# Kernel optimization log

Hardware: AMD Instinct MI355X
Metric: run time of the kernel (lower is better)

Reference implementation:

```python
import jax, jax.numpy as jnp
import numpy as np

EPS = 1e-12  # F.normalize eps


def setup_inputs() -> dict:
    key = jax.random.key(0)
    k1, k2 = jax.random.split(key)
    bs, d = 8192, 128
    data = jax.random.normal(k1, (bs, d), dtype=jnp.float32)
    label = jax.random.randint(k2, (bs, 1), 0, 2, dtype=jnp.int64)
    scale = jnp.asarray(np.log(1.0 / 0.07), dtype=jnp.float32)  # learned temperature param
    return {"data": data, "scale": scale, "label": label}


def reference(data, scale, label):
    bs = data.shape[0]
    # L2-normalize rows (F.normalize semantics with eps clamp)
    norm = jnp.maximum(jnp.linalg.norm(data, axis=-1, keepdims=True), EPS)
    x = data / norm
    logits = (x @ x.T) * jnp.exp(scale)  # [bs, bs]
    # Vectorized equivalent of the python double loop: binary same-class matrix
    sim = (label == label.T).astype(logits.dtype)  # [bs, bs]
    q = jax.nn.softmax(sim / jnp.sum(sim, axis=-1, keepdims=True), axis=-1)
    p = jax.nn.log_softmax(logits, axis=-1)
    log_q = jnp.log(q)  # q > 0 always (softmax output)
    # F.kl_div(p, q, 'batchmean') = sum(q * (log q - p)) / bs
    loss1 = jnp.sum(q * (log_q - p)) / bs
    # F.kl_div(q.log(), p.exp(), 'batchmean') = sum(exp(p) * (p - log q)) / bs
    loss2 = jnp.sum(jnp.exp(p) * (p - log_q)) / bs
    return (loss1 + loss2) * 0.5
```

## Files before the change

kernel.cpp:

```cpp
#include <hip/hip_runtime.h>
#include <stdint.h>

#define BS 8192
#define DD 128
#define L2E 1.4426950408889634f
#define LN2 0.6931471805599453f

typedef __attribute__((ext_vector_type(8))) short short8;
typedef __attribute__((ext_vector_type(4))) float float4v;

#if __has_builtin(__builtin_amdgcn_exp2f)
#define EXP2(x) __builtin_amdgcn_exp2f(x)
#else
#define EXP2(x) exp2f(x)
#endif

__device__ __forceinline__ float bf2f(short s) {
  union { unsigned u; float f; } c;
  c.u = ((unsigned)(unsigned short)s) << 16;
  return c.f;
}
__device__ __forceinline__ short f2bf(float f) {
  union { float f; unsigned u; } c; c.f = f;
  unsigned u = c.u + 0x7FFFu + ((c.u >> 16) & 1u);
  return (short)(u >> 16);
}


__global__ __launch_bounds__(256) void k_norm(const float* __restrict__ data,
                                              const int* __restrict__ label,
                                              char* __restrict__ xnbF,
                                              float* __restrict__ gh16,
                                              float* __restrict__ Zr,
                                              float* __restrict__ Ur,
                                              float* __restrict__ Vr,
                                              float* __restrict__ mf) {
  __shared__ float shg[256];
  int tid = threadIdx.x, wave = tid >> 6, lane = tid & 63;
  int lh = lane & 31, rsel = lane >> 5;
  shg[tid] = 0.f;
  int rowbase = blockIdx.x * 16;
  if (tid < 16) {
    int row = rowbase + tid;
    Zr[row] = 0.f; Ur[row] = 0.f; Vr[row] = 0.f;
    mf[row] = (label[row] == 0) ? 1.f : 0.f;
  }
  __syncthreads();

  float a00 = 0.f, a01 = 0.f, a02 = 0.f, a03 = 0.f;
  float a10 = 0.f, a11 = 0.f, a12 = 0.f, a13 = 0.f;
#pragma unroll
  for (int it = 0; it < 2; ++it) {
    int row = rowbase + it * 8 + wave * 2 + rsel;
    float4 v = *(const float4*)&data[row * DD + lh * 4];
    float ss = v.x * v.x + v.y * v.y + v.z * v.z + v.w * v.w;
#pragma unroll
    for (int off = 16; off; off >>= 1) ss += __shfl_xor(ss, off);
    float rn = 1.f / fmaxf(sqrtf(ss), 1e-12f);
    float x0 = v.x * rn, x1 = v.y * rn, x2 = v.z * rn, x3 = v.w * rn;

    unsigned pk0 = (unsigned)(unsigned short)f2bf(x0) |
                   ((unsigned)(unsigned short)f2bf(x1) << 16);
    unsigned pk1 = (unsigned)(unsigned short)f2bf(x2) |
                   ((unsigned)(unsigned short)f2bf(x3) << 16);
    int kc = lh >> 1;
    size_t chunk = (size_t)(row >> 4) * 256 + (size_t)(kc >> 2) * 64 +
                   (size_t)(kc & 3) * 16 + (row & 15);
    *(uint2*)(xnbF + chunk * 16 + (lh & 1) * 8) = make_uint2(pk0, pk1);

    int lab = label[row];
    if (lab == 0) {
      a00 += x0; a01 += x1; a02 += x2; a03 += x3;
    } else {
      a10 += x0; a11 += x1; a12 += x2; a13 += x3;
    }
  }
  int base = lh * 4;
  atomicAdd(&shg[base + 0], a00); atomicAdd(&shg[base + 1], a01);
  atomicAdd(&shg[base + 2], a02); atomicAdd(&shg[base + 3], a03);
  atomicAdd(&shg[128 + base + 0], a10); atomicAdd(&shg[128 + base + 1], a11);
  atomicAdd(&shg[128 + base + 2], a12); atomicAdd(&shg[128 + base + 3], a13);
  __syncthreads();
  atomicAdd(&gh16[(blockIdx.x & 15) * 256 + tid], shg[tid]);
}

__global__ __launch_bounds__(512, 4) void k_main(const short* __restrict__ xnbF,
                                                 const int* __restrict__ label,
                                                 const float* __restrict__ mf,
                                                 const float* __restrict__ scale,
                                                 const float* __restrict__ gh16,
                                                 float* __restrict__ Zr,
                                                 float* __restrict__ Ur,
                                                 float* __restrict__ Vr,
                                                 int* __restrict__ ticket,
                                                 float* __restrict__ out) {
  __shared__ short tile[2][64 * DD];
  __shared__ int credu[8];
  __shared__ float fredu[8];
  __shared__ float dred[24];
  __shared__ int lastf;
  int tid = threadIdx.x, wave = tid >> 6, lane = tid & 63;
  int quad = lane >> 4, col = lane & 15;
  int rbI = blockIdx.x >> 4;
  int sl = blockIdx.x & 15;
  float se2 = __expf(scale[0]) * L2E;

  const short8* F = (const short8*)xnbF;
  int gA = rbI * 16 + wave * 2;
  short8 af[2][4];
#pragma unroll
  for (int s = 0; s < 2; ++s)
#pragma unroll
    for (int t = 0; t < 4; ++t) {
      short8 a = F[(size_t)(gA + s) * 256 + t * 64 + lane];
#pragma unroll
      for (int i = 0; i < 8; ++i) a[i] = f2bf(bf2f(a[i]) * se2);
      af[s][t] = a;
    }

  float4v Z0 = {0.f,0.f,0.f,0.f}, Z1 = Z0, U0 = Z0, U1 = Z0, V0 = Z0, V1 = Z0;
  int cb4 = sl * 32;

#define STAGE(buf, jt)                                                         \
  {                                                                            \
    const char* s_ = (const char*)xnbF +                                       \
                     ((size_t)(cb4 + (jt) * 4) * 256 + tid) * 16;              \
    char* d_ = (char*)tile[buf] + tid * 16;                                    \
    __builtin_amdgcn_global_load_lds(                                          \
        (const __attribute__((address_space(1))) void*)(uintptr_t)s_,          \
        (__attribute__((address_space(3))) void*)(uintptr_t)d_, 16, 0, 0);     \
    __builtin_amdgcn_global_load_lds(                                          \
        (const __attribute__((address_space(1))) void*)(uintptr_t)(s_ + 8192), \
        (__attribute__((address_space(3))) void*)(uintptr_t)(d_ + 8192),       \
        16, 0, 0);                                                             \
  }

  STAGE(0, 0);
  __syncthreads();

#pragma unroll 1
  for (int jt = 0; jt < 8; ++jt) {
    if (jt < 7) STAGE((jt + 1) & 1, jt + 1);
    const short8* T8 = (const short8*)tile[jt & 1];
    int jcb = sl * 512 + jt * 64;

#define HALFTILE(jo)                                                           \
    {                                                                          \
      short8 b00 = T8[(jo) * 256 + lane];                                      \
      short8 b01 = T8[(jo) * 256 + 64 + lane];                                 \
      short8 b02 = T8[(jo) * 256 + 128 + lane];                                \
      short8 b03 = T8[(jo) * 256 + 192 + lane];                                \
      short8 b10 = T8[(jo + 1) * 256 + lane];                                  \
      short8 b11 = T8[(jo + 1) * 256 + 64 + lane];                             \
      short8 b12 = T8[(jo + 1) * 256 + 128 + lane];                            \
      short8 b13 = T8[(jo + 1) * 256 + 192 + lane];                            \
      float m0 = mf[jcb + (jo) * 16 + col];                                    \
      float m1 = mf[jcb + (jo + 1) * 16 + col];                                \
      float4v c00 = {0.f, 0.f, 0.f, 0.f}, c01 = c00, c10 = c00, c11 = c00;     \
      c00 = __builtin_amdgcn_mfma_f32_16x16x32_bf16(af[0][0], b00, c00, 0,0,0);\
      c01 = __builtin_amdgcn_mfma_f32_16x16x32_bf16(af[1][0], b00, c01, 0,0,0);\
      c10 = __builtin_amdgcn_mfma_f32_16x16x32_bf16(af[0][0], b10, c10, 0,0,0);\
      c11 = __builtin_amdgcn_mfma_f32_16x16x32_bf16(af[1][0], b10, c11, 0,0,0);\
      c00 = __builtin_amdgcn_mfma_f32_16x16x32_bf16(af[0][1], b01, c00, 0,0,0);\
      c01 = __builtin_amdgcn_mfma_f32_16x16x32_bf16(af[1][1], b01, c01, 0,0,0);\
      c10 = __builtin_amdgcn_mfma_f32_16x16x32_bf16(af[0][1], b11, c10, 0,0,0);\
      c11 = __builtin_amdgcn_mfma_f32_16x16x32_bf16(af[1][1], b11, c11, 0,0,0);\
      c00 = __builtin_amdgcn_mfma_f32_16x16x32_bf16(af[0][2], b02, c00, 0,0,0);\
      c01 = __builtin_amdgcn_mfma_f32_16x16x32_bf16(af[1][2], b02, c01, 0,0,0);\
      c10 = __builtin_amdgcn_mfma_f32_16x16x32_bf16(af[0][2], b12, c10, 0,0,0);\
      c11 = __builtin_amdgcn_mfma_f32_16x16x32_bf16(af[1][2], b12, c11, 0,0,0);\
      c00 = __builtin_amdgcn_mfma_f32_16x16x32_bf16(af[0][3], b03, c00, 0,0,0);\
      c01 = __builtin_amdgcn_mfma_f32_16x16x32_bf16(af[1][3], b03, c01, 0,0,0);\
      c10 = __builtin_amdgcn_mfma_f32_16x16x32_bf16(af[0][3], b13, c10, 0,0,0);\
      c11 = __builtin_amdgcn_mfma_f32_16x16x32_bf16(af[1][3], b13, c11, 0,0,0);\
      _Pragma("unroll")                                                        \
      for (int r = 0; r < 4; ++r) {  \
        float l, e;                                                            \
        l = c00[r]; e = EXP2(l);        \
        Z0[r] += e; U0[r] = fmaf(e, l, U0[r]); V0[r] = fmaf(m0, e, V0[r]);     \
        l = c01[r]; e = EXP2(l);                                               \
        Z1[r] += e; U1[r] = fmaf(e, l, U1[r]); V1[r] = fmaf(m0, e, V1[r]);     \
        l = c10[r]; e = EXP2(l);                                               \
        Z0[r] += e; U0[r] = fmaf(e, l, U0[r]); V0[r] = fmaf(m1, e, V0[r]);     \
        l = c11[r]; e = EXP2(l);                                               \
        Z1[r] += e; U1[r] = fmaf(e, l, U1[r]); V1[r] = fmaf(m1, e, V1[r]);     \
      }                                                                        \
    }
    HALFTILE(0)
    HALFTILE(2)
#undef HALFTILE
    __syncthreads();
  }
#undef STAGE

#define EMIT(s, Zc, Uc, Vc)                                                    \
  {                                                                            \
    _Pragma("unroll")                                                          \
    for (int r = 0; r < 4; ++r) {                                              \
      float z = Zc[r], u = Uc[r], v0 = Vc[r];                                  \
      _Pragma("unroll")                                                        \
      for (int off = 1; off < 16; off <<= 1) {                                 \
        z += __shfl_xor(z, off);                                               \
        u += __shfl_xor(u, off);                                               \
        v0 += __shfl_xor(v0, off);                                             \
      }                                                                        \
      if (col == 0) {                                                          \
        int row = rbI * 256 + wave * 32 + s * 16 + quad * 4 + r;               \
        int lab = label[row];                                                  \
        float v = (lab == 0) ? v0 : (z - v0);                                  \
        atomicAdd(&Zr[row], z);                                                \
        atomicAdd(&Ur[row], u * LN2);                 \
        atomicAdd(&Vr[row], v);                                                \
      }                                                                        \
    }                                                                          \
  }
  EMIT(0, Z0, U0, V0)
  EMIT(1, Z1, U1, V1)
#undef EMIT

  __syncthreads();
  if (tid == 0) {
    int t = __hip_atomic_fetch_add(ticket, 1, __ATOMIC_ACQ_REL,
                                   __HIP_MEMORY_SCOPE_AGENT);
    lastf = (t == 511);
  }
  __syncthreads();
  if (!lastf) return;

  float* hs = (float*)tile;
  if (tid < 256) {
    float h = 0.f;
#pragma unroll
    for (int i = 0; i < 16; ++i) h += gh16[i * 256 + tid];
    hs[tid] = h;
  }
  int c1i = 0;
#pragma unroll
  for (int k = 0; k < 16; ++k) c1i += label[k * 512 + tid];
#pragma unroll
  for (int off = 32; off; off >>= 1) c1i += __shfl_xor(c1i, off);
  if (lane == 0) credu[wave] = c1i;
  __syncthreads();
  int c1t = 0;
#pragma unroll
  for (int w = 0; w < 8; ++w) c1t += credu[w];
  float c1 = (float)c1t, c0 = (float)(BS - c1t);

  float p00 = 0.f, p01 = 0.f, p11 = 0.f;
  if (tid < 128) {
    float h0d = hs[tid], h1d = hs[128 + tid];
    p00 = h0d * h0d; p01 = h0d * h1d; p11 = h1d * h1d;
  }
#pragma unroll
  for (int off = 32; off; off >>= 1) {
    p00 += __shfl_xor(p00, off);
    p01 += __shfl_xor(p01, off);
    p11 += __shfl_xor(p11, off);
  }
  if (lane == 0) { dred[wave] = p00; dred[8 + wave] = p01; dred[16 + wave] = p11; }

  float rc0 = 1.f / c0, rc1 = 1.f / c1;
  float local = 0.f;
#pragma unroll
  for (int k = 0; k < 16; ++k) {
    int row = k * 512 + tid;
    int lab = label[row];
    float Z = __hip_atomic_load(&Zr[row], __ATOMIC_RELAXED, __HIP_MEMORY_SCOPE_AGENT);
    float U = __hip_atomic_load(&Ur[row], __ATOMIC_RELAXED, __HIP_MEMORY_SCOPE_AGENT);
    float V = __hip_atomic_load(&Vr[row], __ATOMIC_RELAXED, __HIP_MEMORY_SCOPE_AGENT);
    local += (U - V * (lab ? rc1 : rc0)) / Z;
  }
#pragma unroll
  for (int off = 32; off; off >>= 1) local += __shfl_xor(local, off);
  if (lane == 0) fredu[wave] = local;
  __syncthreads();
  if (tid == 0) {
    float se = __expf(scale[0]);
    float a0 = __expf(1.f / c0), a1 = __expf(1.f / c1);
    float rZq0 = 1.f / (c0 * a0 + ((float)BS - c0));
    float rZq1 = 1.f / (c1 * a1 + ((float)BS - c1));
    float d00 = dred[0] + dred[1], d01 = dred[8] + dred[9],
          d11 = dred[16] + dred[17];
    float rows = 0.f;
#pragma unroll
    for (int w = 0; w < 8; ++w) rows += fredu[w];
    float stsum = se * (rZq0 * ((d00 + d01) + (a0 - 1.f) * d00) +
                        rZq1 * ((d01 + d11) + (a1 - 1.f) * d11));
    float total = c0 * a0 * rZq0 + c1 * a1 * rZq1 - stsum + rows;
    out[0] = total * (0.5f / (float)BS);
  }
}

extern "C" void kernel_launch(void* const* d_in, const int* in_sizes, int n_in,
                              void* d_out, int out_size, void* d_ws, size_t ws_size,
                              hipStream_t stream) {
  const float* data = (const float*)d_in[0];
  const float* scale = (const float*)d_in[1];
  const int* label = (const int*)d_in[2];
  char* ws = (char*)d_ws;
  char* xnbF = ws;
  float* Zr = (float*)(ws + 2097152);
  float* Ur = (float*)(ws + 2129920);
  float* Vr = (float*)(ws + 2162688);
  float* gh16 = (float*)(ws + 2195456);
  int* ticket = (int*)(ws + 2211840);
  float* mf = (float*)(ws + 2211872);

  hipMemsetAsync(ws + 2195456, 0, 16388, stream);

  k_norm<<<512, 256, 0, stream>>>(data, label, xnbF, gh16, Zr, Ur, Vr, mf);
  k_main<<<512, 512, 0, stream>>>((const short*)xnbF, label, mf, scale, gh16,
                                  Zr, Ur, Vr, ticket, (float*)d_out);
}
```

Measured before the change: 102.9 us.

## Replace memset and ticket-based last-block finalize with separate finalize kernel

```diff
diff --git a/kernel.cpp b/kernel.cpp
--- a/kernel.cpp
+++ b/kernel.cpp
@@ -30,7 +30,7 @@
 __global__ __launch_bounds__(256) void k_norm(const float* __restrict__ data,
                                               const int* __restrict__ label,
                                               char* __restrict__ xnbF,
-                                              float* __restrict__ gh16,
+                                              float* __restrict__ gpart,
                                               float* __restrict__ Zr,
                                               float* __restrict__ Ur,
                                               float* __restrict__ Vr,
@@ -39,8 +39,8 @@
   int tid = threadIdx.x, wave = tid >> 6, lane = tid & 63;
   int lh = lane & 31, rsel = lane >> 5;
   shg[tid] = 0.f;
-  int rowbase = blockIdx.x * 16;
-  if (tid < 16) {
+  int rowbase = blockIdx.x * 64;
+  if (tid < 64) {
     int row = rowbase + tid;
     Zr[row] = 0.f; Ur[row] = 0.f; Vr[row] = 0.f;
     mf[row] = (label[row] == 0) ? 1.f : 0.f;
@@ -50,7 +50,7 @@
   float a00 = 0.f, a01 = 0.f, a02 = 0.f, a03 = 0.f;
   float a10 = 0.f, a11 = 0.f, a12 = 0.f, a13 = 0.f;
 #pragma unroll
-  for (int it = 0; it < 2; ++it) {
+  for (int it = 0; it < 8; ++it) {
     int row = rowbase + it * 8 + wave * 2 + rsel;
     float4 v = *(const float4*)&data[row * DD + lh * 4];
     float ss = v.x * v.x + v.y * v.y + v.z * v.z + v.w * v.w;
@@ -81,24 +81,17 @@
   atomicAdd(&shg[128 + base + 0], a10); atomicAdd(&shg[128 + base + 1], a11);
   atomicAdd(&shg[128 + base + 2], a12); atomicAdd(&shg[128 + base + 3], a13);
   __syncthreads();
-  atomicAdd(&gh16[(blockIdx.x & 15) * 256 + tid], shg[tid]);
+  gpart[blockIdx.x * 256 + tid] = shg[tid];
 }
 
 __global__ __launch_bounds__(512, 4) void k_main(const short* __restrict__ xnbF,
                                                  const int* __restrict__ label,
                                                  const float* __restrict__ mf,
                                                  const float* __restrict__ scale,
-                                                 const float* __restrict__ gh16,
                                                  float* __restrict__ Zr,
                                                  float* __restrict__ Ur,
-                                                 float* __restrict__ Vr,
-                                                 int* __restrict__ ticket,
-                                                 float* __restrict__ out) {
+                                                 float* __restrict__ Vr) {
   __shared__ short tile[2][64 * DD];
-  __shared__ int credu[8];
-  __shared__ float fredu[8];
-  __shared__ float dred[24];
-  __shared__ int lastf;
   int tid = threadIdx.x, wave = tid >> 6, lane = tid & 63;
   int quad = lane >> 4, col = lane & 15;
   int rbI = blockIdx.x >> 4;
@@ -217,21 +210,25 @@
   EMIT(0, Z0, U0, V0)
   EMIT(1, Z1, U1, V1)
 #undef EMIT
-
-  __syncthreads();
-  if (tid == 0) {
-    int t = __hip_atomic_fetch_add(ticket, 1, __ATOMIC_ACQ_REL,
-                                   __HIP_MEMORY_SCOPE_AGENT);
-    lastf = (t == 511);
-  }
-  __syncthreads();
-  if (!lastf) return;
-
-  float* hs = (float*)tile;
+}
+
+__global__ __launch_bounds__(512) void k_fin(const int* __restrict__ label,
+                                             const float* __restrict__ scale,
+                                             const float* __restrict__ gpart,
+                                             const float* __restrict__ Zr,
+                                             const float* __restrict__ Ur,
+                                             const float* __restrict__ Vr,
+                                             float* __restrict__ out) {
+  __shared__ float hs[256];
+  __shared__ int credu[8];
+  __shared__ float fredu[8];
+  __shared__ float dred[24];
+  int tid = threadIdx.x, wave = tid >> 6, lane = tid & 63;
+
   if (tid < 256) {
     float h = 0.f;
-#pragma unroll
-    for (int i = 0; i < 16; ++i) h += gh16[i * 256 + tid];
+#pragma unroll 8
+    for (int b = 0; b < 128; ++b) h += gpart[b * 256 + tid];
     hs[tid] = h;
   }
   int c1i = 0;
@@ -265,10 +262,7 @@
   for (int k = 0; k < 16; ++k) {
     int row = k * 512 + tid;
     int lab = label[row];
-    float Z = __hip_atomic_load(&Zr[row], __ATOMIC_RELAXED, __HIP_MEMORY_SCOPE_AGENT);
-    float U = __hip_atomic_load(&Ur[row], __ATOMIC_RELAXED, __HIP_MEMORY_SCOPE_AGENT);
-    float V = __hip_atomic_load(&Vr[row], __ATOMIC_RELAXED, __HIP_MEMORY_SCOPE_AGENT);
-    local += (U - V * (lab ? rc1 : rc0)) / Z;
+    local += (Ur[row] - Vr[row] * (lab ? rc1 : rc0)) / Zr[row];
   }
 #pragma unroll
   for (int off = 32; off; off >>= 1) local += __shfl_xor(local, off);
@@ -302,13 +296,10 @@
   float* Zr = (float*)(ws + 2097152);
   float* Ur = (float*)(ws + 2129920);
   float* Vr = (float*)(ws + 2162688);
-  float* gh16 = (float*)(ws + 2195456);
-  int* ticket = (int*)(ws + 2211840);
-  float* mf = (float*)(ws + 2211872);
-
-  hipMemsetAsync(ws + 2195456, 0, 16388, stream);
-
-  k_norm<<<512, 256, 0, stream>>>(data, label, xnbF, gh16, Zr, Ur, Vr, mf);
-  k_main<<<512, 512, 0, stream>>>((const short*)xnbF, label, mf, scale, gh16,
-                                  Zr, Ur, Vr, ticket, (float*)d_out);
-}
+  float* gpart = (float*)(ws + 2195456);
+  float* mf = (float*)(ws + 2326528);
+
+  k_norm<<<128, 256, 0, stream>>>(data, label, xnbF, gpart, Zr, Ur, Vr, mf);
+  k_main<<<512, 512, 0, stream>>>((const short*)xnbF, label, mf, scale, Zr, Ur, Vr);
+  k_fin<<<1, 512, 0, stream>>>(label, scale, gpart, Zr, Ur, Vr, (float*)d_out);
+}
```

New measurement: 108.0 us. +5.0%, slower.
